# Optimization experiments

Measured on AMD Instinct MI355X. Metric: run time of the kernel, lower is better.

## Reference

```python
import jax, jax.numpy as jnp
import numpy as np

N, H, W = 4, 96, 96
C, G, K = 128, 8, 3
GC = C // G          # group channels = 16
P = K * K            # sampling points per group = 9
PAD = K // 2
OFS = 1.0            # offset_scale
HID = 4 * C          # mlp hidden
EPS = 1e-5           # torch nn.LayerNorm default eps


def _ln(x, g, b):
    m = jnp.mean(x, -1, keepdims=True)
    v = jnp.mean((x - m) ** 2, -1, keepdims=True)
    return (x - m) * jax.lax.rsqrt(v + EPS) * g + b


def _dcnv3_core(x, offset, mask):
    # x: (n,H,W,C) channels-last, offset: (n,H,W,G*P*2), mask: (n,H,W,G,P) softmaxed.
    # Faithful port of dcnv3_core_pytorch (stride=1, dilation=1, zero-pad grid_sample,
    # align_corners=False -> pixel = loc*size - 0.5).
    n = x.shape[0]
    xp = jnp.pad(x, ((0, 0), (PAD, PAD), (PAD, PAD), (0, 0)))
    Hin, Win = H + 2 * PAD, W + 2 * PAD
    L = H * W
    base = (K - 1) // 2 + 0.5
    ref_x = (base + jnp.arange(W, dtype=x.dtype)) / Win  # normalized by padded size
    ref_y = (base + jnp.arange(H, dtype=x.dtype)) / Hin
    k = jnp.arange(K, dtype=x.dtype) - (K - 1) // 2
    dx = jnp.repeat(k, K) / Win  # torch meshgrid('ij'): kernel-x varies slowest
    dy = jnp.tile(k, K) / Hin
    off = offset.reshape(n, H, W, G, P, 2)
    # absolute sampling pixel coords (grid_sample align_corners=False)
    px = (ref_x[None, None, :, None, None] + dx * OFS + off[..., 0] * OFS / Win) * Win - 0.5
    py = (ref_y[None, :, None, None, None] + dy * OFS + off[..., 1] * OFS / Hin) * Hin - 0.5
    # layout (n,G,L,P)
    px = px.transpose(0, 3, 1, 2, 4).reshape(n, G, L, P)
    py = py.transpose(0, 3, 1, 2, 4).reshape(n, G, L, P)
    mk = mask.transpose(0, 3, 1, 2, 4).reshape(n, G, L, P)
    xg = xp.reshape(n, Hin * Win, G, GC).transpose(0, 2, 1, 3)
    x0 = jnp.floor(px); y0 = jnp.floor(py)
    fx = px - x0; fy = py - y0
    x0 = x0.astype(jnp.int32); y0 = y0.astype(jnp.int32)
    x1 = x0 + 1; y1 = y0 + 1
    out = jnp.zeros((n, G, L, GC), x.dtype)
    for yi, xi, w in ((y0, x0, (1 - fy) * (1 - fx)), (y0, x1, (1 - fy) * fx),
                      (y1, x0, fy * (1 - fx)), (y1, x1, fy * fx)):
        valid = (yi >= 0) & (yi < Hin) & (xi >= 0) & (xi < Win)
        idx = jnp.clip(yi, 0, Hin - 1) * Win + jnp.clip(xi, 0, Win - 1)
        v = jnp.take_along_axis(xg, idx.reshape(n, G, L * P, 1), axis=2)
        v = v.reshape(n, G, L, P, GC)
        out = out + jnp.einsum('nglp,nglpc->nglc', jnp.where(valid, w, 0.0) * mk, v)
    return out.transpose(0, 2, 1, 3).reshape(n, H, W, C)


def _dcn(x, w_in, b_in, dw_k, dw_b, dwg, dwb, w_off, b_off, w_msk, b_msk, w_out, b_out):
    n = x.shape[0]
    xproj = x @ w_in + b_in
    x1 = jax.lax.conv_general_dilated(
        x, dw_k, (1, 1), 'SAME',
        dimension_numbers=('NHWC', 'HWIO', 'NHWC'),
        feature_group_count=C) + dw_b
    x1 = jax.nn.gelu(_ln(x1, dwg, dwb), approximate=False)
    offset = x1 @ w_off + b_off
    mask = jax.nn.softmax((x1 @ w_msk + b_msk).reshape(n, H, W, G, P), axis=-1)
    y = _dcnv3_core(xproj, offset, mask)
    return y @ w_out + b_out


def setup_inputs() -> dict:
    key = jax.random.key(0)
    ks = jax.random.split(key, 10)
    rn = lambda k, s, sc: jax.random.normal(k, s, jnp.float32) * sc
    return {
        'x': rn(ks[0], (N, H, W, C), 1.0),
        'ln1g': jnp.ones((C,), jnp.float32), 'ln1b': jnp.zeros((C,), jnp.float32),
        'w_in': rn(ks[1], (C, C), 0.02), 'b_in': jnp.zeros((C,), jnp.float32),
        'dw_k': rn(ks[2], (K, K, 1, C), 0.1), 'dw_b': jnp.zeros((C,), jnp.float32),
        'dwg': jnp.ones((C,), jnp.float32), 'dwb': jnp.zeros((C,), jnp.float32),
        'w_off': rn(ks[3], (C, G * P * 2), 0.01), 'b_off': rn(ks[4], (G * P * 2,), 0.1),
        'w_msk': rn(ks[5], (C, G * P), 0.02), 'b_msk': jnp.zeros((G * P,), jnp.float32),
        'w_out': rn(ks[6], (C, C), 0.02), 'b_out': jnp.zeros((C,), jnp.float32),
        'ln2g': jnp.ones((C,), jnp.float32), 'ln2b': jnp.zeros((C,), jnp.float32),
        'w1': rn(ks[7], (C, HID), 0.02), 'b1': jnp.zeros((HID,), jnp.float32),
        'w2': rn(ks[8], (HID, C), 0.02), 'b2': jnp.zeros((C,), jnp.float32),
    }


def reference(x, ln1g, ln1b, w_in, b_in, dw_k, dw_b, dwg, dwb, w_off, b_off,
              w_msk, b_msk, w_out, b_out, ln2g, ln2b, w1, b1, w2, b2):
    # pre-norm InternImage block: x = x + dcn(LN1(x)); x = x + mlp(LN2(x))
    x = x + _dcn(_ln(x, ln1g, ln1b), w_in, b_in, dw_k, dw_b, dwg, dwb,
                 w_off, b_off, w_msk, b_msk, w_out, b_out)
    h = _ln(x, ln2g, ln2b)
    h = jax.nn.gelu(h @ w1 + b1, approximate=False) @ w2 + b2
    return x + h
```

## Files before the change

kernel.cpp:

```cpp
#include <hip/hip_runtime.h>
#include <hip/hip_bf16.h>
#include <math.h>

using bf16 = __hip_bfloat16;
using bf162 = __hip_bfloat162;

typedef __bf16 bf16x8 __attribute__((ext_vector_type(8)));
typedef float floatx4 __attribute__((ext_vector_type(4)));

constexpr int NB = 4, HH = 96, WW = 96, CC = 128, GG = 8, PP = 9;
constexpr int HW = HH * WW;
constexpr int NPIX = NB * HW;

__device__ __forceinline__ float ld1(const float* p) { return *p; }
__device__ __forceinline__ float ld1(const bf16* p)  { return __bfloat162float(*p); }
__device__ __forceinline__ void st1(float* p, float v) { *p = v; }
__device__ __forceinline__ void st1(bf16* p, float v)  { *p = __float2bfloat16(v); }
__device__ __forceinline__ float b2f(bf16 v) { return __bfloat162float(v); }
__device__ __forceinline__ bf16 f2b(float v) { return __float2bfloat16(v); }
__device__ __forceinline__ float gelu_exact(float v) {
    return 0.5f * v * (1.0f + erff(v * 0.7071067811865475f));
}
__device__ __forceinline__ floatx4 MFMA(bf16x8 a, bf16x8 b, floatx4 c) {
    return __builtin_amdgcn_mfma_f32_16x16x32_bf16(a, b, c, 0, 0, 0);
}

struct PrepArgs {
    const float* src[6];
    bf16* dst[6];
    int K[6], N[6];
    int cum[7];
    const float* b_off; const float* b_msk; float* b_om;
};

__global__ __launch_bounds__(256) void prep_weights(PrepArgs pa, int total)
{
    int t = blockIdx.x * 256 + threadIdx.x;
    if (t >= total) return;
    if (t >= pa.cum[6]) {
        int e = t - pa.cum[6];
        pa.b_om[e] = (e < 144) ? pa.b_off[e] : pa.b_msk[e - 144];
        return;
    }
    int i = 0;
    #pragma unroll
    for (int j = 0; j < 5; ++j) if (t >= pa.cum[j + 1]) i = j + 1;
    int e = t - pa.cum[i];
    int Ki = pa.K[i], Ni = pa.N[i];
    int n = e / Ki, k = e - n * Ki;
    pa.dst[i][e] = f2b(pa.src[i][(size_t)k * Ni + n]);
}

template<typename TI, typename TO>
__global__ __launch_bounds__(256) void ln_kernel(
    const TI* __restrict__ X, const float* __restrict__ g,
    const float* __restrict__ b, TO* __restrict__ out)
{
    int wave = (blockIdx.x * 256 + threadIdx.x) >> 6;
    int lane = threadIdx.x & 63;
    if (wave >= NPIX) return;
    const TI* xp = X + (size_t)wave * 128 + 2 * lane;
    float v0 = ld1(xp), v1 = ld1(xp + 1);
    float s = v0 + v1, q = v0 * v0 + v1 * v1;
    #pragma unroll
    for (int o = 32; o; o >>= 1) { s += __shfl_xor(s, o); q += __shfl_xor(q, o); }
    float mean = s * (1.0f / 128.0f);
    float rstd = rsqrtf(q * (1.0f / 128.0f) - mean * mean + 1e-5f);
    float g0 = g[2 * lane], g1 = g[2 * lane + 1];
    float b0 = b[2 * lane], b1 = b[2 * lane + 1];
    TO* op = out + (size_t)wave * 128 + 2 * lane;
    st1(op,     (v0 - mean) * rstd * g0 + b0);
    st1(op + 1, (v1 - mean) * rstd * g1 + b1);
}

__global__ __launch_bounds__(256) void dwconv_ln_gelu_kernel(
    const bf16* __restrict__ xln, const float* __restrict__ dwk,
    const float* __restrict__ dwb, const float* __restrict__ gam,
    const float* __restrict__ bet, bf16* __restrict__ out)
{
    int wave = (blockIdx.x * 256 + threadIdx.x) >> 6;
    int lane = threadIdx.x & 63;
    if (wave >= NPIX) return;
    int n = wave / HW; int rem = wave % HW;
    int y = rem / WW;  int x = rem % WW;
    const bf162* xp = (const bf162*)xln;
    float a0 = 0.f, a1 = 0.f;
    #pragma unroll
    for (int ky = 0; ky < 3; ++ky) {
        int yy = y + ky - 1;
        if (yy < 0 || yy >= HH) continue;
        #pragma unroll
        for (int kx = 0; kx < 3; ++kx) {
            int xx = x + kx - 1;
            if (xx < 0 || xx >= WW) continue;
            bf162 v = xp[((size_t)(n * HH + yy) * WW + xx) * 64 + lane];
            const float* w = dwk + (ky * 3 + kx) * CC + 2 * lane;
            a0 = fmaf(b2f(v.x), w[0], a0);
            a1 = fmaf(b2f(v.y), w[1], a1);
        }
    }
    a0 += dwb[2 * lane]; a1 += dwb[2 * lane + 1];
    float s = a0 + a1, q = a0 * a0 + a1 * a1;
    #pragma unroll
    for (int o = 32; o; o >>= 1) { s += __shfl_xor(s, o); q += __shfl_xor(q, o); }
    float mean = s * (1.0f / 128.0f);
    float rstd = rsqrtf(q * (1.0f / 128.0f) - mean * mean + 1e-5f);
    float h0 = gelu_exact((a0 - mean) * rstd * gam[2 * lane]     + bet[2 * lane]);
    float h1 = gelu_exact((a1 - mean) * rstd * gam[2 * lane + 1] + bet[2 * lane + 1]);
    bf162 o2; o2.x = f2b(h0); o2.y = f2b(h1);
    ((bf162*)out)[(size_t)wave * 64 + lane] = o2;
}

__global__ __launch_bounds__(256) void dcn_core_kernel(
    const bf16* __restrict__ xproj, const bf16* __restrict__ omr,
    bf16* __restrict__ out)
{
    __shared__ int4   sOff[4][72];
    __shared__ float4 sW[4][72];
    __shared__ float  sRaw[4][72];
    int wv = threadIdx.x >> 6;
    int lane = threadIdx.x & 63;
    int pix = blockIdx.x * 4 + wv;
    int n = pix / HW; int rem = pix % HW;
    int iy = rem / WW; int ix = rem % WW;
    const bf16* om = omr + (size_t)pix * 216;

    for (int e = lane; e < 72; e += 64)
        sRaw[wv][e] = b2f(om[144 + e]);
    __syncthreads();

    for (int e = lane; e < 72; e += 64) {
        int g = e / 9, p = e - 9 * g;
        float mx = -1e30f;
        #pragma unroll
        for (int i = 0; i < 9; ++i) mx = fmaxf(mx, sRaw[wv][g * 9 + i]);
        float ssum = 0.f;
        #pragma unroll
        for (int i = 0; i < 9; ++i) ssum += __expf(sRaw[wv][g * 9 + i] - mx);
        float mw = __expf(sRaw[wv][e] - mx) / ssum;

        float ox = b2f(om[g * 18 + 2 * p]);
        float oy = b2f(om[g * 18 + 2 * p + 1]);
        int kx = p / 3 - 1, ky = p % 3 - 1;
        float px = (float)(ix + kx) + ox;
        float py = (float)(iy + ky) + oy;
        float fx0 = floorf(px), fy0 = floorf(py);
        int x0 = (int)fx0, y0 = (int)fy0;
        float fx = px - fx0, fy = py - fy0;
        bool vx0 = (x0 >= 0) & (x0 < WW), vx1 = (x0 + 1 >= 0) & (x0 + 1 < WW);
        bool vy0 = (y0 >= 0) & (y0 < HH), vy1 = (y0 + 1 >= 0) & (y0 + 1 < HH);
        float w00 = (1.f - fy) * (1.f - fx) * mw * (vy0 && vx0 ? 1.f : 0.f);
        float w01 = (1.f - fy) * fx         * mw * (vy0 && vx1 ? 1.f : 0.f);
        float w10 = fy * (1.f - fx)         * mw * (vy1 && vx0 ? 1.f : 0.f);
        float w11 = fy * fx                 * mw * (vy1 && vx1 ? 1.f : 0.f);
        int x0c = min(max(x0, 0), WW - 1), x1c = min(max(x0 + 1, 0), WW - 1);
        int y0c = min(max(y0, 0), HH - 1), y1c = min(max(y0 + 1, 0), HH - 1);
        sOff[wv][e] = make_int4((y0c * WW + x0c) * CC, (y0c * WW + x1c) * CC,
                                (y1c * WW + x0c) * CC, (y1c * WW + x1c) * CC);
        sW[wv][e] = make_float4(w00, w01, w10, w11);
    }
    __syncthreads();

    const bf16* xb = xproj + (size_t)n * HW * CC + 2 * lane;
    int gbase = (lane >> 3) * 9;
    float a0 = 0.f, a1 = 0.f;
    #pragma unroll
    for (int p = 0; p < 9; ++p) {
        int4 o = sOff[wv][gbase + p];
        float4 w = sW[wv][gbase + p];
        bf162 v00 = *(const bf162*)(xb + o.x);
        bf162 v01 = *(const bf162*)(xb + o.y);
        bf162 v10 = *(const bf162*)(xb + o.z);
        bf162 v11 = *(const bf162*)(xb + o.w);
        a0 += w.x * b2f(v00.x) + w.y * b2f(v01.x) + w.z * b2f(v10.x) + w.w * b2f(v11.x);
        a1 += w.x * b2f(v00.y) + w.y * b2f(v01.y) + w.z * b2f(v10.y) + w.w * b2f(v11.y);
    }
    bf162 o2; o2.x = f2b(a0); o2.y = f2b(a1);
    ((bf162*)out)[(size_t)pix * 64 + lane] = o2;
}

__global__ __launch_bounds__(256) void gemm_mfma_kernel(
    const bf16* __restrict__ A, const bf16* __restrict__ Wt,
    const float* __restrict__ bias, bf16* __restrict__ Out, int M, int Nn, int K)
{
    __shared__ __align__(16) __bf16 As[64][72];
    __shared__ __align__(16) __bf16 Bs[64][72];
    int tid = threadIdx.x;
    int wv = tid >> 6, lane = tid & 63;
    int bm = blockIdx.y * 64, bn = blockIdx.x * 64;
    int mI = lane & 15, q = lane >> 4;
    floatx4 acc[4] = {};

    for (int k0 = 0; k0 < K; k0 += 64) {
        #pragma unroll
        for (int cc = 0; cc < 2; ++cc) {
            int ch = tid * 2 + cc;
            int row = ch >> 3, ko = (ch & 7) * 8;
            *reinterpret_cast<uint4*>(&As[row][ko]) =
                *reinterpret_cast<const uint4*>(A + (size_t)(bm + row) * K + k0 + ko);
            int ng = bn + row;
            uint4 bv = make_uint4(0, 0, 0, 0);
            if (ng < Nn) bv = *reinterpret_cast<const uint4*>(Wt + (size_t)ng * K + k0 + ko);
            *reinterpret_cast<uint4*>(&Bs[row][ko]) = bv;
        }
        __syncthreads();
        #pragma unroll
        for (int kk = 0; kk < 64; kk += 32) {
            bf16x8 a = *reinterpret_cast<const bf16x8*>(&As[wv * 16 + mI][kk + q * 8]);
            #pragma unroll
            for (int t = 0; t < 4; ++t) {
                bf16x8 b = *reinterpret_cast<const bf16x8*>(&Bs[t * 16 + mI][kk + q * 8]);
                acc[t] = MFMA(a, b, acc[t]);
            }
        }
        __syncthreads();
    }
    int row0 = bm + wv * 16 + q * 4;
    #pragma unroll
    for (int t = 0; t < 4; ++t) {
        int col = bn + t * 16 + mI;
        if (col >= Nn) continue;
        float bs = bias[col];
        #pragma unroll
        for (int r = 0; r < 4; ++r)
            st1(Out + (size_t)(row0 + r) * Nn + col, acc[t][r] + bs);
    }
}

__global__ __launch_bounds__(256, 3) void fused_tail_kernel(
    const bf16* __restrict__ ycore, const float* __restrict__ x,
    const bf16* __restrict__ w_outT, const float* __restrict__ b_out,
    const float* __restrict__ ln2g, const float* __restrict__ ln2b,
    const bf16* __restrict__ w1T, const float* __restrict__ b1,
    const bf16* __restrict__ w2T, const float* __restrict__ b2,
    float* __restrict__ out)
{
    __shared__ __align__(16) bf16 sA[64 * 136];
    __shared__ __align__(16) bf16 sXres[64 * 136];
    __shared__ __align__(16) bf16 sH2[64 * 136];
    int tid = threadIdx.x, wv = tid >> 6, lane = tid & 63;
    int mI = lane & 15, q = lane >> 4;
    int bm = blockIdx.x * 64;

    bf16x8 bw0[4][2];
    #pragma unroll
    for (int ks = 0; ks < 4; ++ks)
        #pragma unroll
        for (int ct = 0; ct < 2; ++ct)
            bw0[ks][ct] = *reinterpret_cast<const bf16x8*>(
                w_outT + (size_t)(wv * 32 + ct * 16 + mI) * 128 + ks * 32 + q * 8);

    #pragma unroll
    for (int i = 0; i < 4; ++i) {
        int s = tid + 256 * i;
        int row = s >> 4, ko = (s & 15) * 8;
        *reinterpret_cast<uint4*>(&sA[row * 136 + ko]) =
            *reinterpret_cast<const uint4*>(ycore + (size_t)(bm + row) * 128 + ko);
    }
    __syncthreads();

    floatx4 acc0[4][2] = {};
    #pragma unroll
    for (int ks = 0; ks < 4; ++ks) {
        int k = ks * 32 + q * 8;
        bf16x8 a[4];
        #pragma unroll
        for (int rt = 0; rt < 4; ++rt)
            a[rt] = *reinterpret_cast<const bf16x8*>(&sA[(rt * 16 + mI) * 136 + k]);
        #pragma unroll
        for (int ct = 0; ct < 2; ++ct)
            #pragma unroll
            for (int rt = 0; rt < 4; ++rt)
                acc0[rt][ct] = MFMA(a[rt], bw0[ks][ct], acc0[rt][ct]);
    }
    #pragma unroll
    for (int rt = 0; rt < 4; ++rt)
        #pragma unroll
        for (int ct = 0; ct < 2; ++ct) {
            int col = wv * 32 + ct * 16 + mI;
            float bs = b_out[col];
            #pragma unroll
            for (int r = 0; r < 4; ++r) {
                int row = rt * 16 + q * 4 + r;
                float v = acc0[rt][ct][r] + bs + x[(size_t)(bm + row) * 128 + col];
                sXres[row * 136 + col] = f2b(v);
            }
        }
    __syncthreads();

    {
        int row = tid >> 2, part = tid & 3;
        float s = 0.f, sq = 0.f;
        float vals[32];
        #pragma unroll
        for (int j = 0; j < 4; ++j) {
            bf16x8 v = *reinterpret_cast<const bf16x8*>(&sXres[row * 136 + part * 32 + j * 8]);
            #pragma unroll
            for (int e = 0; e < 8; ++e) {
                float f = (float)v[e];
                vals[j * 8 + e] = f; s += f; sq += f * f;
            }
        }
        s  += __shfl_xor(s, 1);  s += __shfl_xor(s, 2);
        sq += __shfl_xor(sq, 1); sq += __shfl_xor(sq, 2);
        float mean = s * (1.0f / 128.0f);
        float rstd = rsqrtf(sq * (1.0f / 128.0f) - mean * mean + 1e-5f);
        #pragma unroll
        for (int j = 0; j < 4; ++j) {
            bf16x8 o;
            #pragma unroll
            for (int e = 0; e < 8; ++e) {
                int ch = part * 32 + j * 8 + e;
                bf16 t = f2b((vals[j * 8 + e] - mean) * rstd * ln2g[ch] + ln2b[ch]);
                o[e] = *reinterpret_cast<__bf16*>(&t);
            }
            *reinterpret_cast<bf16x8*>(&sH2[row * 136 + part * 32 + j * 8]) = o;
        }
    }
    __syncthreads();

    floatx4 acc2[4][2] = {};
    #pragma unroll 1
    for (int ph = 0; ph < 4; ++ph) {
        bf16x8 bw1[4][2];
        #pragma unroll
        for (int ks = 0; ks < 4; ++ks)
            #pragma unroll
            for (int ct = 0; ct < 2; ++ct)
                bw1[ks][ct] = *reinterpret_cast<const bf16x8*>(
                    w1T + (size_t)(ph * 128 + wv * 32 + ct * 16 + mI) * 128 + ks * 32 + q * 8);
        floatx4 acc1[4][2] = {};
        #pragma unroll
        for (int ks = 0; ks < 4; ++ks) {
            int k = ks * 32 + q * 8;
            bf16x8 a[4];
            #pragma unroll
            for (int rt = 0; rt < 4; ++rt)
                a[rt] = *reinterpret_cast<const bf16x8*>(&sH2[(rt * 16 + mI) * 136 + k]);
            #pragma unroll
            for (int ct = 0; ct < 2; ++ct)
                #pragma unroll
                for (int rt = 0; rt < 4; ++rt)
                    acc1[rt][ct] = MFMA(a[rt], bw1[ks][ct], acc1[rt][ct]);
        }
        __syncthreads();
        bf16x8 bw2[4][2];
        #pragma unroll
        for (int ks = 0; ks < 4; ++ks)
            #pragma unroll
            for (int ct = 0; ct < 2; ++ct)
                bw2[ks][ct] = *reinterpret_cast<const bf16x8*>(
                    w2T + (size_t)(wv * 32 + ct * 16 + mI) * 512 + ph * 128 + ks * 32 + q * 8);
        #pragma unroll
        for (int rt = 0; rt < 4; ++rt)
            #pragma unroll
            for (int ct = 0; ct < 2; ++ct) {
                int lcol = wv * 32 + ct * 16 + mI;
                float bs = b1[ph * 128 + lcol];
                #pragma unroll
                for (int r = 0; r < 4; ++r) {
                    int row = rt * 16 + q * 4 + r;
                    sA[row * 136 + lcol] = f2b(gelu_exact(acc1[rt][ct][r] + bs));
                }
            }
        __syncthreads();
        #pragma unroll
        for (int ks = 0; ks < 4; ++ks) {
            int k = ks * 32 + q * 8;
            bf16x8 a[4];
            #pragma unroll
            for (int rt = 0; rt < 4; ++rt)
                a[rt] = *reinterpret_cast<const bf16x8*>(&sA[(rt * 16 + mI) * 136 + k]);
            #pragma unroll
            for (int ct = 0; ct < 2; ++ct)
                #pragma unroll
                for (int rt = 0; rt < 4; ++rt)
                    acc2[rt][ct] = MFMA(a[rt], bw2[ks][ct], acc2[rt][ct]);
        }
    }
    #pragma unroll
    for (int rt = 0; rt < 4; ++rt)
        #pragma unroll
        for (int ct = 0; ct < 2; ++ct) {
            int col = wv * 32 + ct * 16 + mI;
            float bs = b2[col];
            #pragma unroll
            for (int r = 0; r < 4; ++r) {
                int row = rt * 16 + q * 4 + r;
                out[(size_t)(bm + row) * 128 + col] =
                    acc2[rt][ct][r] + bs + b2f(sXres[row * 136 + col]);
            }
        }
}

extern "C" void kernel_launch(void* const* d_in, const int* in_sizes, int n_in,
                              void* d_out, int out_size, void* d_ws, size_t ws_size,
                              hipStream_t stream)
{
    const float* x     = (const float*)d_in[0];
    const float* ln1g  = (const float*)d_in[1];
    const float* ln1b  = (const float*)d_in[2];
    const float* w_in  = (const float*)d_in[3];
    const float* b_in  = (const float*)d_in[4];
    const float* dw_k  = (const float*)d_in[5];
    const float* dw_b  = (const float*)d_in[6];
    const float* dwg   = (const float*)d_in[7];
    const float* dwb   = (const float*)d_in[8];
    const float* w_off = (const float*)d_in[9];
    const float* b_off = (const float*)d_in[10];
    const float* w_msk = (const float*)d_in[11];
    const float* b_msk = (const float*)d_in[12];
    const float* w_out = (const float*)d_in[13];
    const float* b_out = (const float*)d_in[14];
    const float* ln2g  = (const float*)d_in[15];
    const float* ln2b  = (const float*)d_in[16];
    const float* w1    = (const float*)d_in[17];
    const float* b1    = (const float*)d_in[18];
    const float* w2    = (const float*)d_in[19];
    const float* b2    = (const float*)d_in[20];
    float* out = (float*)d_out;

    bf16* ws = (bf16*)d_ws;
    bf16* xln   = ws;
    bf16* xproj = xln   + (size_t)NPIX * 128;
    bf16* x1    = xproj + (size_t)NPIX * 128;
    bf16* omr   = x1    + (size_t)NPIX * 128;
    bf16* ycore = xln;
    bf16* wT    = ws + (size_t)NPIX * 600;
    bf16* w_inT  = wT;
    bf16* w_omT  = w_inT  + 16384;
    bf16* w_outT = w_omT  + 27648;
    bf16* w1T    = w_outT + 16384;
    bf16* w2T    = w1T    + 65536;
    float* b_om  = (float*)(w2T + 65536);
    const int WTOT = 191488 + 216;

    PrepArgs pa;
    pa.src[0] = w_in;  pa.dst[0] = w_inT;            pa.K[0] = 128; pa.N[0] = 128;
    pa.src[1] = w_off; pa.dst[1] = w_omT;            pa.K[1] = 128; pa.N[1] = 144;
    pa.src[2] = w_msk; pa.dst[2] = w_omT + 144*128;  pa.K[2] = 128; pa.N[2] = 72;
    pa.src[3] = w_out; pa.dst[3] = w_outT;           pa.K[3] = 128; pa.N[3] = 128;
    pa.src[4] = w1;    pa.dst[4] = w1T;              pa.K[4] = 128; pa.N[4] = 512;
    pa.src[5] = w2;    pa.dst[5] = w2T;              pa.K[5] = 512; pa.N[5] = 128;
    pa.cum[0] = 0;     pa.cum[1] = 16384;  pa.cum[2] = 34816; pa.cum[3] = 44032;
    pa.cum[4] = 60416; pa.cum[5] = 125952; pa.cum[6] = 191488;
    pa.b_off = b_off;  pa.b_msk = b_msk;   pa.b_om = b_om;

    const int M = NPIX;
    dim3 blk(256);

    prep_weights<<<(WTOT + 255) / 256, blk, 0, stream>>>(pa, WTOT);
    ln_kernel<float, bf16><<<NPIX / 4, blk, 0, stream>>>(x, ln1g, ln1b, xln);
    gemm_mfma_kernel<<<dim3(2, M / 64), blk, 0, stream>>>(
        xln, w_inT, b_in, xproj, M, 128, 128);
    dwconv_ln_gelu_kernel<<<NPIX / 4, blk, 0, stream>>>(xln, dw_k, dw_b, dwg, dwb, x1);
    gemm_mfma_kernel<<<dim3(4, M / 64), blk, 0, stream>>>(
        x1, w_omT, b_om, omr, M, 216, 128);
    dcn_core_kernel<<<NPIX / 4, blk, 0, stream>>>(xproj, omr, ycore);
    fused_tail_kernel<<<M / 64, blk, 0, stream>>>(
        ycore, x, w_outT, b_out, ln2g, ln2b, w1T, b1, w2T, b2, out);
}
```

Baseline: 236.0 us.

## Restructure MLP tail so each wave owns 16 rows, removing block barriers

The fused MLP in the tail kernel is reorganised. Before, the four waves split output columns and exchanged hidden activations through a shared 64x128 tile, which needed block-wide barriers in every phase. Now each wave owns 16 rows and loops over 16 hidden chunks of 32 columns. It writes GELU output into a private double-buffered LDS strip and immediately multiplies it by W2, so only wave-local ordering (an lgkmcnt wait) is required. This removes __syncthreads and frees LDS, but each wave now loads all W1 and W2 weights from global or L2 memory itself, raising weight traffic fourfold per block.

```diff
diff --git a/kernel.cpp b/kernel.cpp
--- a/kernel.cpp
+++ b/kernel.cpp
@@ -235,9 +235,9 @@
     const bf16* __restrict__ w2T, const float* __restrict__ b2,
     float* __restrict__ out)
 {
-    __shared__ __align__(16) bf16 sA[64 * 136];
+    __shared__ __align__(16) bf16 sStage[64 * 136];
     __shared__ __align__(16) bf16 sXres[64 * 136];
-    __shared__ __align__(16) bf16 sH2[64 * 136];
+    __shared__ __align__(16) bf16 sP[4][2][16 * 40];
     int tid = threadIdx.x, wv = tid >> 6, lane = tid & 63;
     int mI = lane & 15, q = lane >> 4;
     int bm = blockIdx.x * 64;
@@ -254,7 +254,7 @@
     for (int i = 0; i < 4; ++i) {
         int s = tid + 256 * i;
         int row = s >> 4, ko = (s & 15) * 8;
-        *reinterpret_cast<uint4*>(&sA[row * 136 + ko]) =
+        *reinterpret_cast<uint4*>(&sStage[row * 136 + ko]) =
             *reinterpret_cast<const uint4*>(ycore + (size_t)(bm + row) * 128 + ko);
     }
     __syncthreads();
@@ -266,7 +266,7 @@
         bf16x8 a[4];
         #pragma unroll
         for (int rt = 0; rt < 4; ++rt)
-            a[rt] = *reinterpret_cast<const bf16x8*>(&sA[(rt * 16 + mI) * 136 + k]);
+            a[rt] = *reinterpret_cast<const bf16x8*>(&sStage[(rt * 16 + mI) * 136 + k]);
         #pragma unroll
         for (int ct = 0; ct < 2; ++ct)
             #pragma unroll
@@ -314,83 +314,73 @@
                 bf16 t = f2b((vals[j * 8 + e] - mean) * rstd * ln2g[ch] + ln2b[ch]);
                 o[e] = *reinterpret_cast<__bf16*>(&t);
             }
-            *reinterpret_cast<bf16x8*>(&sH2[row * 136 + part * 32 + j * 8]) = o;
+            *reinterpret_cast<bf16x8*>(&sStage[row * 136 + part * 32 + j * 8]) = o;
         }
     }
     __syncthreads();
 
-    floatx4 acc2[4][2] = {};
-    #pragma unroll 1
-    for (int ph = 0; ph < 4; ++ph) {
-        bf16x8 bw1[4][2];
+    const bf16* sH2row = &sStage[(wv * 16 + mI) * 136];
+    bf16* myP[2] = { &sP[wv][0][0], &sP[wv][1][0] };
+    floatx4 acc2[8] = {};
+
+    bf16x8 bw1[4][2];
+    #pragma unroll
+    for (int ks = 0; ks < 4; ++ks)
+        #pragma unroll
+        for (int ct = 0; ct < 2; ++ct)
+            bw1[ks][ct] = *reinterpret_cast<const bf16x8*>(
+                w1T + (size_t)(ct * 16 + mI) * 128 + ks * 32 + q * 8);
+
+    #pragma unroll 2
+    for (int c = 0; c < 16; ++c) {
+        bf16* strip = myP[c & 1];
+        bf16x8 a1[4];
         #pragma unroll
         for (int ks = 0; ks < 4; ++ks)
+            a1[ks] = *reinterpret_cast<const bf16x8*>(sH2row + ks * 32 + q * 8);
+        floatx4 acc1[2] = {};
+        #pragma unroll
+        for (int ks = 0; ks < 4; ++ks)
             #pragma unroll
             for (int ct = 0; ct < 2; ++ct)
-                bw1[ks][ct] = *reinterpret_cast<const bf16x8*>(
-                    w1T + (size_t)(ph * 128 + wv * 32 + ct * 16 + mI) * 128 + ks * 32 + q * 8);
-        floatx4 acc1[4][2] = {};
-        #pragma unroll
-        for (int ks = 0; ks < 4; ++ks) {
-            int k = ks * 32 + q * 8;
-            bf16x8 a[4];
-            #pragma unroll
-            for (int rt = 0; rt < 4; ++rt)
-                a[rt] = *reinterpret_cast<const bf16x8*>(&sH2[(rt * 16 + mI) * 136 + k]);
-            #pragma unroll
-            for (int ct = 0; ct < 2; ++ct)
+                acc1[ct] = MFMA(a1[ks], bw1[ks][ct], acc1[ct]);
+        bf16x8 bw2[8];
+        #pragma unroll
+        for (int ct2 = 0; ct2 < 8; ++ct2)
+            bw2[ct2] = *reinterpret_cast<const bf16x8*>(
+                w2T + (size_t)(ct2 * 16 + mI) * 512 + c * 32 + q * 8);
+        float b1v0 = b1[c * 32 + mI], b1v1 = b1[c * 32 + 16 + mI];
+        #pragma unroll
+        for (int r = 0; r < 4; ++r) {
+            strip[(q * 4 + r) * 40 + mI]      = f2b(gelu_exact(acc1[0][r] + b1v0));
+            strip[(q * 4 + r) * 40 + 16 + mI] = f2b(gelu_exact(acc1[1][r] + b1v1));
+        }
+        if (c < 15) {
+            #pragma unroll
+            for (int ks = 0; ks < 4; ++ks)
                 #pragma unroll
-                for (int rt = 0; rt < 4; ++rt)
-                    acc1[rt][ct] = MFMA(a[rt], bw1[ks][ct], acc1[rt][ct]);
-        }
-        __syncthreads();
-        bf16x8 bw2[4][2];
-        #pragma unroll
-        for (int ks = 0; ks < 4; ++ks)
-            #pragma unroll
-            for (int ct = 0; ct < 2; ++ct)
-                bw2[ks][ct] = *reinterpret_cast<const bf16x8*>(
-                    w2T + (size_t)(wv * 32 + ct * 16 + mI) * 512 + ph * 128 + ks * 32 + q * 8);
-        #pragma unroll
-        for (int rt = 0; rt < 4; ++rt)
-            #pragma unroll
-            for (int ct = 0; ct < 2; ++ct) {
-                int lcol = wv * 32 + ct * 16 + mI;
-                float bs = b1[ph * 128 + lcol];
-                #pragma unroll
-                for (int r = 0; r < 4; ++r) {
-                    int row = rt * 16 + q * 4 + r;
-                    sA[row * 136 + lcol] = f2b(gelu_exact(acc1[rt][ct][r] + bs));
-                }
-            }
-        __syncthreads();
-        #pragma unroll
-        for (int ks = 0; ks < 4; ++ks) {
-            int k = ks * 32 + q * 8;
-            bf16x8 a[4];
-            #pragma unroll
-            for (int rt = 0; rt < 4; ++rt)
-                a[rt] = *reinterpret_cast<const bf16x8*>(&sA[(rt * 16 + mI) * 136 + k]);
-            #pragma unroll
-            for (int ct = 0; ct < 2; ++ct)
-                #pragma unroll
-                for (int rt = 0; rt < 4; ++rt)
-                    acc2[rt][ct] = MFMA(a[rt], bw2[ks][ct], acc2[rt][ct]);
-        }
-    }
-    #pragma unroll
-    for (int rt = 0; rt < 4; ++rt)
-        #pragma unroll
-        for (int ct = 0; ct < 2; ++ct) {
-            int col = wv * 32 + ct * 16 + mI;
-            float bs = b2[col];
-            #pragma unroll
-            for (int r = 0; r < 4; ++r) {
-                int row = rt * 16 + q * 4 + r;
-                out[(size_t)(bm + row) * 128 + col] =
-                    acc2[rt][ct][r] + bs + b2f(sXres[row * 136 + col]);
-            }
-        }
+                for (int ct = 0; ct < 2; ++ct)
+                    bw1[ks][ct] = *reinterpret_cast<const bf16x8*>(
+                        w1T + (size_t)((c + 1) * 32 + ct * 16 + mI) * 128 + ks * 32 + q * 8);
+        }
+        asm volatile("s_waitcnt lgkmcnt(0)" ::: "memory");
+        bf16x8 a2 = *reinterpret_cast<const bf16x8*>(&strip[mI * 40 + q * 8]);
+        #pragma unroll
+        for (int ct2 = 0; ct2 < 8; ++ct2)
+            acc2[ct2] = MFMA(a2, bw2[ct2], acc2[ct2]);
+    }
+
+    #pragma unroll
+    for (int ct2 = 0; ct2 < 8; ++ct2) {
+        int col = ct2 * 16 + mI;
+        float bs = b2[col];
+        #pragma unroll
+        for (int r = 0; r < 4; ++r) {
+            int row = wv * 16 + q * 4 + r;
+            out[(size_t)(bm + row) * 128 + col] =
+                acc2[ct2][r] + bs + b2f(sXres[row * 136 + col]);
+        }
+    }
 }
 
 extern "C" void kernel_launch(void* const* d_in, const int* in_sizes, int n_in,
```

Result: slower. 292.0 us (+23.8%).

## Keep tail residual in registers, double-buffer GELU tile, prefetch next w1

Applied to the files above, without the earlier changes.

The fused tail kernel now keeps the post-DCN residual in fp32 registers instead of a bf16 shared tile. It computes the LN2 row statistics directly from the MFMA output layout, using shuffles and a small shared partial-sum array, which removes the separate LDS round-trip. The GELU hidden tile is double-buffered so one barrier per MLP phase can be dropped, and the next phase's w1 fragments are prefetched while the current GELU is written out. This trims shared-memory traffic and synchronisation, but raises register pressure at launch bounds 256,3 and slightly changes numerics because the residual is no longer rounded to bf16.

```diff
diff --git a/kernel.cpp b/kernel.cpp
--- a/kernel.cpp
+++ b/kernel.cpp
@@ -235,9 +235,10 @@
     const bf16* __restrict__ w2T, const float* __restrict__ b2,
     float* __restrict__ out)
 {
-    __shared__ __align__(16) bf16 sA[64 * 136];
-    __shared__ __align__(16) bf16 sXres[64 * 136];
-    __shared__ __align__(16) bf16 sH2[64 * 136];
+    __shared__ __align__(16) bf16 sStage[64 * 136];
+    __shared__ __align__(16) bf16 sH1[2][64 * 136];
+    float* sLN = (float*)&sH1[1][0];
+
     int tid = threadIdx.x, wv = tid >> 6, lane = tid & 63;
     int mI = lane & 15, q = lane >> 4;
     int bm = blockIdx.x * 64;
@@ -254,7 +255,7 @@
     for (int i = 0; i < 4; ++i) {
         int s = tid + 256 * i;
         int row = s >> 4, ko = (s & 15) * 8;
-        *reinterpret_cast<uint4*>(&sA[row * 136 + ko]) =
+        *reinterpret_cast<uint4*>(&sStage[row * 136 + ko]) =
             *reinterpret_cast<const uint4*>(ycore + (size_t)(bm + row) * 128 + ko);
     }
     __syncthreads();
@@ -266,69 +267,84 @@
         bf16x8 a[4];
         #pragma unroll
         for (int rt = 0; rt < 4; ++rt)
-            a[rt] = *reinterpret_cast<const bf16x8*>(&sA[(rt * 16 + mI) * 136 + k]);
+            a[rt] = *reinterpret_cast<const bf16x8*>(&sStage[(rt * 16 + mI) * 136 + k]);
         #pragma unroll
         for (int ct = 0; ct < 2; ++ct)
             #pragma unroll
             for (int rt = 0; rt < 4; ++rt)
                 acc0[rt][ct] = MFMA(a[rt], bw0[ks][ct], acc0[rt][ct]);
     }
+
+    float xr[4][2][4];
+    float psum[4][4], psq[4][4];
     #pragma unroll
     for (int rt = 0; rt < 4; ++rt)
         #pragma unroll
-        for (int ct = 0; ct < 2; ++ct) {
-            int col = wv * 32 + ct * 16 + mI;
-            float bs = b_out[col];
+        for (int r = 0; r < 4; ++r) {
+            int row = rt * 16 + q * 4 + r;
+            float v0 = acc0[rt][0][r] + b_out[wv * 32 + mI]
+                     + x[(size_t)(bm + row) * 128 + wv * 32 + mI];
+            float v1 = acc0[rt][1][r] + b_out[wv * 32 + 16 + mI]
+                     + x[(size_t)(bm + row) * 128 + wv * 32 + 16 + mI];
+            xr[rt][0][r] = v0; xr[rt][1][r] = v1;
+            psum[rt][r] = v0 + v1;
+            psq[rt][r]  = v0 * v0 + v1 * v1;
+        }
+    #pragma unroll
+    for (int o = 1; o < 16; o <<= 1)
+        #pragma unroll
+        for (int rt = 0; rt < 4; ++rt)
+            #pragma unroll
+            for (int r = 0; r < 4; ++r) {
+                psum[rt][r] += __shfl_xor(psum[rt][r], o);
+                psq[rt][r]  += __shfl_xor(psq[rt][r], o);
+            }
+    if (mI == 0) {
+        #pragma unroll
+        for (int rt = 0; rt < 4; ++rt)
             #pragma unroll
             for (int r = 0; r < 4; ++r) {
                 int row = rt * 16 + q * 4 + r;
-                float v = acc0[rt][ct][r] + bs + x[(size_t)(bm + row) * 128 + col];
-                sXres[row * 136 + col] = f2b(v);
-            }
-        }
+                sLN[row * 8 + wv * 2]     = psum[rt][r];
+                sLN[row * 8 + wv * 2 + 1] = psq[rt][r];
+            }
+    }
     __syncthreads();
 
     {
-        int row = tid >> 2, part = tid & 3;
-        float s = 0.f, sq = 0.f;
-        float vals[32];
-        #pragma unroll
-        for (int j = 0; j < 4; ++j) {
-            bf16x8 v = *reinterpret_cast<const bf16x8*>(&sXres[row * 136 + part * 32 + j * 8]);
-            #pragma unroll
-            for (int e = 0; e < 8; ++e) {
-                float f = (float)v[e];
-                vals[j * 8 + e] = f; s += f; sq += f * f;
-            }
-        }
-        s  += __shfl_xor(s, 1);  s += __shfl_xor(s, 2);
-        sq += __shfl_xor(sq, 1); sq += __shfl_xor(sq, 2);
-        float mean = s * (1.0f / 128.0f);
-        float rstd = rsqrtf(sq * (1.0f / 128.0f) - mean * mean + 1e-5f);
-        #pragma unroll
-        for (int j = 0; j < 4; ++j) {
-            bf16x8 o;
-            #pragma unroll
-            for (int e = 0; e < 8; ++e) {
-                int ch = part * 32 + j * 8 + e;
-                bf16 t = f2b((vals[j * 8 + e] - mean) * rstd * ln2g[ch] + ln2b[ch]);
-                o[e] = *reinterpret_cast<__bf16*>(&t);
-            }
-            *reinterpret_cast<bf16x8*>(&sH2[row * 136 + part * 32 + j * 8]) = o;
-        }
+        float g0 = ln2g[wv * 32 + mI],      g1 = ln2g[wv * 32 + 16 + mI];
+        float be0 = ln2b[wv * 32 + mI],     be1 = ln2b[wv * 32 + 16 + mI];
+        #pragma unroll
+        for (int rt = 0; rt < 4; ++rt)
+            #pragma unroll
+            for (int r = 0; r < 4; ++r) {
+                int row = rt * 16 + q * 4 + r;
+                float4 p0 = *reinterpret_cast<float4*>(&sLN[row * 8]);
+                float4 p1 = *reinterpret_cast<float4*>(&sLN[row * 8 + 4]);
+                float s  = p0.x + p0.z + p1.x + p1.z;
+                float sq = p0.y + p0.w + p1.y + p1.w;
+                float mean = s * (1.0f / 128.0f);
+                float rstd = rsqrtf(sq * (1.0f / 128.0f) - mean * mean + 1e-5f);
+                sStage[row * 136 + wv * 32 + mI] =
+                    f2b((xr[rt][0][r] - mean) * rstd * g0 + be0);
+                sStage[row * 136 + wv * 32 + 16 + mI] =
+                    f2b((xr[rt][1][r] - mean) * rstd * g1 + be1);
+            }
     }
     __syncthreads();
 
     floatx4 acc2[4][2] = {};
+    bf16x8 bw1[4][2];
+    #pragma unroll
+    for (int ks = 0; ks < 4; ++ks)
+        #pragma unroll
+        for (int ct = 0; ct < 2; ++ct)
+            bw1[ks][ct] = *reinterpret_cast<const bf16x8*>(
+                w1T + (size_t)(wv * 32 + ct * 16 + mI) * 128 + ks * 32 + q * 8);
+
     #pragma unroll 1
     for (int ph = 0; ph < 4; ++ph) {
-        bf16x8 bw1[4][2];
-        #pragma unroll
-        for (int ks = 0; ks < 4; ++ks)
-            #pragma unroll
-            for (int ct = 0; ct < 2; ++ct)
-                bw1[ks][ct] = *reinterpret_cast<const bf16x8*>(
-                    w1T + (size_t)(ph * 128 + wv * 32 + ct * 16 + mI) * 128 + ks * 32 + q * 8);
+        bf16* buf = (ph & 1) ? &sH1[1][0] : &sH1[0][0];
         floatx4 acc1[4][2] = {};
         #pragma unroll
         for (int ks = 0; ks < 4; ++ks) {
@@ -336,14 +352,13 @@
             bf16x8 a[4];
             #pragma unroll
             for (int rt = 0; rt < 4; ++rt)
-                a[rt] = *reinterpret_cast<const bf16x8*>(&sH2[(rt * 16 + mI) * 136 + k]);
+                a[rt] = *reinterpret_cast<const bf16x8*>(&sStage[(rt * 16 + mI) * 136 + k]);
             #pragma unroll
             for (int ct = 0; ct < 2; ++ct)
                 #pragma unroll
                 for (int rt = 0; rt < 4; ++rt)
                     acc1[rt][ct] = MFMA(a[rt], bw1[ks][ct], acc1[rt][ct]);
         }
-        __syncthreads();
         bf16x8 bw2[4][2];
         #pragma unroll
         for (int ks = 0; ks < 4; ++ks)
@@ -360,9 +375,18 @@
                 #pragma unroll
                 for (int r = 0; r < 4; ++r) {
                     int row = rt * 16 + q * 4 + r;
-                    sA[row * 136 + lcol] = f2b(gelu_exact(acc1[rt][ct][r] + bs));
+                    buf[row * 136 + lcol] = f2b(gelu_exact(acc1[rt][ct][r] + bs));
                 }
             }
+        if (ph < 3) {
+            #pragma unroll
+            for (int ks = 0; ks < 4; ++ks)
+                #pragma unroll
+                for (int ct = 0; ct < 2; ++ct)
+                    bw1[ks][ct] = *reinterpret_cast<const bf16x8*>(
+                        w1T + (size_t)((ph + 1) * 128 + wv * 32 + ct * 16 + mI) * 128
+                            + ks * 32 + q * 8);
+        }
         __syncthreads();
         #pragma unroll
         for (int ks = 0; ks < 4; ++ks) {
@@ -370,7 +394,7 @@
             bf16x8 a[4];
             #pragma unroll
             for (int rt = 0; rt < 4; ++rt)
-                a[rt] = *reinterpret_cast<const bf16x8*>(&sA[(rt * 16 + mI) * 136 + k]);
+                a[rt] = *reinterpret_cast<const bf16x8*>(&buf[(rt * 16 + mI) * 136 + k]);
             #pragma unroll
             for (int ct = 0; ct < 2; ++ct)
                 #pragma unroll
@@ -388,7 +412,7 @@
             for (int r = 0; r < 4; ++r) {
                 int row = rt * 16 + q * 4 + r;
                 out[(size_t)(bm + row) * 128 + col] =
-                    acc2[rt][ct][r] + bs + b2f(sXres[row * 136 + col]);
+                    acc2[rt][ct][r] + bs + xr[rt][ct][r];
             }
         }
 }
```

Result: slower. 254.7 us (+7.9%).
